# Performance work log

Measured on AMD Instinct MI355X. Metric: run time of the kernel, lower is better.

The kernel has to match this reference:

```python
import jax, jax.numpy as jnp
import numpy as np

B, H, S = 32, 128, 8192

def setup_inputs() -> dict:
    key = jax.random.key(0)
    k1, k2, k3, k4, k5 = jax.random.split(key, 5)
    return {
        "static_hidden": jax.random.normal(k1, (B, H, S), dtype=jnp.float32),
        "dynamic_hidden": jax.random.normal(k2, (B, H, S), dtype=jnp.float32),
        "decoder_hidden": jax.random.normal(k3, (B, H), dtype=jnp.float32),
        "v": jax.random.normal(k4, (1, 1, H), dtype=jnp.float32) * 0.01,
        "W": jax.random.normal(k5, (1, H, 3 * H), dtype=jnp.float32) * 0.01,
    }

def reference(static_hidden, dynamic_hidden, decoder_hidden, v, W):
    b, h, s = static_hidden.shape
    # concat (static, dynamic, expanded decoder) along feature dim -> [b, 3h, s]
    hidden = jnp.concatenate(
        [static_hidden, dynamic_hidden,
         jnp.broadcast_to(decoder_hidden[:, :, None], (b, h, s))], axis=1)
    # W[0]: [h, 3h]; tanh(W @ hidden) -> [b, h, s]
    e = jnp.tanh(jnp.einsum('hk,bks->bhs', W[0], hidden))
    # v[0,0]: [h]; scores -> [b, 1, s]
    scores = jnp.einsum('h,bhs->bs', v[0, 0], e)[:, None, :]
    return jax.nn.softmax(scores, axis=2)
```

## Files before the change

kernel.cpp:

```cpp
#include <hip/hip_runtime.h>
#include <math.h>

#define BB 32
#define HH 128
#define SS 8192

typedef __attribute__((ext_vector_type(8))) short bf8;
typedef __attribute__((ext_vector_type(4))) float f4;

static __device__ __forceinline__ unsigned short f2bf(float x) {
  union { float f; unsigned int u; } c; c.f = x;
  unsigned int r = c.u + 0x7FFFu + ((c.u >> 16) & 1u);
  return (unsigned short)(r >> 16);
}

__global__ __launch_bounds__(256) void prep_kernel(
    const float* __restrict__ W, const float* __restrict__ dec,
    unsigned short* __restrict__ Abf, float* __restrict__ bias) {
  const int b = blockIdx.x;
  const int tid = threadIdx.x;
  if (tid < HH) {
    const float* wr = W + (size_t)tid * 384 + 256;
    const float* db = dec + (size_t)b * HH;
    float acc = 0.f;
    #pragma unroll 8
    for (int j = 0; j < HH; ++j) acc += wr[j] * db[j];
    bias[b * HH + tid] = acc;
  }
  if (b == 0) {
    for (int idx = tid; idx < HH * 256; idx += 256) {
      int h = idx >> 8, k = idx & 255;
      Abf[idx] = f2bf(W[h * 384 + k]);
    }
  }
}

__global__ __launch_bounds__(512, 4) void attn_main(
    const float* __restrict__ sta, const float* __restrict__ dyn,
    const unsigned short* __restrict__ Abf, const float* __restrict__ bias,
    const float* __restrict__ v, float* __restrict__ scores) {
  __shared__ unsigned short LA[128 * 256];

  const int tid  = threadIdx.x;
  const int l    = tid & 63;
  const int quad = l >> 4;
  const int n16  = l & 15;
  const int gw   = (blockIdx.x << 3) + (tid >> 6);
  const int b    = gw >> 9;
  const int tile = gw & 511;
  const int s0   = tile << 4;

  #pragma unroll
  for (int j = 0; j < 8; ++j) {
    int gc = (j << 9) + tid;
    int m = gc >> 5, ck = gc & 31;
    bf8 val = *(const bf8*)(Abf + ((size_t)gc << 3));
    *(bf8*)&LA[m * 256 + ((ck ^ (m & 7)) << 3)] = val;
  }
  __syncthreads();

  const size_t base = ((size_t)b << 20) + (size_t)(quad << 3) * SS + s0 + n16;
  const float* p0 = sta + base;
  const float* p1 = dyn + base;

  f4 acc[8];
  #pragma unroll
  for (int mt = 0; mt < 8; ++mt) acc[mt] = (f4){0.f, 0.f, 0.f, 0.f};

  float tmp[8];
  bf8 cur;

  auto issueB = [&](int step) {
    const float* tp = (step < 4 ? p0 : p1) + ((size_t)((step & 3) << 5)) * SS;
    #pragma unroll
    for (int j = 0; j < 8; ++j)
      tmp[j] = tp[(size_t)j * SS];
  };
  auto conv = [&]() {
    #pragma unroll
    for (int j = 0; j < 8; ++j) cur[j] = (short)f2bf(tmp[j]);
  };

  const int swz = n16 & 7;
  issueB(0);
  conv();
  #pragma unroll
  for (int step = 0; step < 8; ++step) {
    if (step < 7) issueB(step + 1);
    const int koff = (((step << 2) + quad) ^ swz) << 3;
    #pragma unroll
    for (int mt = 0; mt < 8; ++mt) {
      bf8 af = *(const bf8*)&LA[(((mt << 4) + n16) << 8) + koff];
      acc[mt] = __builtin_amdgcn_mfma_f32_16x16x32_bf16(af, cur, acc[mt], 0, 0, 0);
    }
    if (step < 7) conv();
  }

  float part = 0.f;
  #pragma unroll
  for (int mt = 0; mt < 8; ++mt) {
    #pragma unroll
    for (int r = 0; r < 4; ++r) {
      const int h = mt * 16 + quad * 4 + r;
      part += v[h] * tanhf(acc[mt][r] + bias[(b << 7) + h]);
    }
  }
  part += __shfl_xor(part, 16, 64);
  part += __shfl_xor(part, 32, 64);
  if (quad == 0)
    scores[((size_t)b << 13) + s0 + n16] = part;
}

__global__ __launch_bounds__(1024) void softmax_kernel(float* __restrict__ out) {
  const int b = blockIdx.x;
  const int tid = threadIdx.x;
  float* row = out + ((size_t)b << 13);
  float4 x0 = ((const float4*)row)[tid];
  float4 x1 = ((const float4*)row)[tid + 1024];
  float lmax = fmaxf(fmaxf(fmaxf(x0.x, x0.y), fmaxf(x0.z, x0.w)),
                     fmaxf(fmaxf(x1.x, x1.y), fmaxf(x1.z, x1.w)));
  __shared__ float red[17];
  #pragma unroll
  for (int o = 32; o >= 1; o >>= 1) lmax = fmaxf(lmax, __shfl_xor(lmax, o, 64));
  if ((tid & 63) == 0) red[tid >> 6] = lmax;
  __syncthreads();
  if (tid < 64) {
    float m = (tid < 16) ? red[tid] : -3.0e38f;
    #pragma unroll
    for (int o = 8; o >= 1; o >>= 1) m = fmaxf(m, __shfl_xor(m, o, 64));
    if (tid == 0) red[16] = m;
  }
  __syncthreads();
  const float gmax = red[16];
  float e[8];
  e[0] = expf(x0.x - gmax); e[1] = expf(x0.y - gmax);
  e[2] = expf(x0.z - gmax); e[3] = expf(x0.w - gmax);
  e[4] = expf(x1.x - gmax); e[5] = expf(x1.y - gmax);
  e[6] = expf(x1.z - gmax); e[7] = expf(x1.w - gmax);
  float ls = e[0] + e[1] + e[2] + e[3] + e[4] + e[5] + e[6] + e[7];
  #pragma unroll
  for (int o = 32; o >= 1; o >>= 1) ls += __shfl_xor(ls, o, 64);
  __syncthreads();
  if ((tid & 63) == 0) red[tid >> 6] = ls;
  __syncthreads();
  if (tid < 64) {
    float m = (tid < 16) ? red[tid] : 0.f;
    #pragma unroll
    for (int o = 8; o >= 1; o >>= 1) m += __shfl_xor(m, o, 64);
    if (tid == 0) red[16] = m;
  }
  __syncthreads();
  const float inv = 1.0f / red[16];
  float4 o0 = make_float4(e[0] * inv, e[1] * inv, e[2] * inv, e[3] * inv);
  float4 o1 = make_float4(e[4] * inv, e[5] * inv, e[6] * inv, e[7] * inv);
  ((float4*)row)[tid] = o0;
  ((float4*)row)[tid + 1024] = o1;
}

extern "C" void kernel_launch(void* const* d_in, const int* in_sizes, int n_in,
                              void* d_out, int out_size, void* d_ws, size_t ws_size,
                              hipStream_t stream) {
  const float* sta = (const float*)d_in[0];
  const float* dyn = (const float*)d_in[1];
  const float* dec = (const float*)d_in[2];
  const float* v   = (const float*)d_in[3];
  const float* W   = (const float*)d_in[4];

  unsigned short* Abf = (unsigned short*)d_ws;
  float* bias = (float*)((char*)d_ws + 128 * 256 * 2);
  float* scores = (float*)d_out;

  prep_kernel<<<BB, 256, 0, stream>>>(W, dec, Abf, bias);
  attn_main<<<BB * (SS / 16) / 8, 512, 0, stream>>>(sta, dyn, Abf, bias, v, scores);
  softmax_kernel<<<BB, 1024, 0, stream>>>(scores);
}
```

Before: 330.9 us.

## Stage activations through double-buffered LDS with vectorized float4 loads

The main kernel now uses 1024-thread blocks, each covering 256 sequence positions. Activations are loaded as float4 vectors, converted to bf16 and written into a swizzled, double-buffered LDS tile, replacing the earlier per-lane scalar strided global loads. MFMA B operands are then read from LDS, with the next chunk's global loads overlapping the current chunk's compute. The cost is 128KB of dynamic shared memory per block, which limits occupancy to one block per CU, plus a block-wide barrier on every chunk.

```diff
diff --git a/kernel.cpp b/kernel.cpp
--- a/kernel.cpp
+++ b/kernel.cpp
@@ -35,65 +35,80 @@
   }
 }
 
-__global__ __launch_bounds__(512, 4) void attn_main(
+__global__ __launch_bounds__(1024, 4) void attn_main(
     const float* __restrict__ sta, const float* __restrict__ dyn,
     const unsigned short* __restrict__ Abf, const float* __restrict__ bias,
     const float* __restrict__ v, float* __restrict__ scores) {
-  __shared__ unsigned short LA[128 * 256];
+  extern __shared__ __align__(16) unsigned short smem[];
+  unsigned short* LA = smem;
+  unsigned short* LX = smem + 32768;
 
   const int tid  = threadIdx.x;
   const int l    = tid & 63;
+  const int w    = tid >> 6;
   const int quad = l >> 4;
   const int n16  = l & 15;
-  const int gw   = (blockIdx.x << 3) + (tid >> 6);
-  const int b    = gw >> 9;
-  const int tile = gw & 511;
-  const int s0   = tile << 4;
+  const int b     = blockIdx.x >> 5;
+  const int s_blk = (blockIdx.x & 31) << 8;
 
+  const int kq = ((w >> 2) << 4) + (quad << 2);
+  const int sl = ((w & 3) << 6) + (n16 << 2);
+  const size_t gxoff = ((size_t)b * HH) * SS + s_blk + sl;
+
+  f4 g[4];
+  auto issueX = [&](int c) {
+    const float* p = (c < 2 ? sta : dyn) + gxoff + (size_t)(((c & 1) << 6) + kq) * SS;
+    #pragma unroll
+    for (int j = 0; j < 4; ++j) g[j] = *(const f4*)(p + (size_t)j * SS);
+  };
+  auto convWrite = [&](int buf) {
+    unsigned short* X = LX + (buf << 14);
+    #pragma unroll
+    for (int i = 0; i < 4; ++i) {
+      const int srow = sl + i;
+      ushort4 o;
+      o.x = f2bf(g[0][i]); o.y = f2bf(g[1][i]);
+      o.z = f2bf(g[2][i]); o.w = f2bf(g[3][i]);
+      *(ushort4*)&X[(srow << 6) + ((((kq >> 3) ^ (srow & 7)) << 3) | (kq & 7))] = o;
+    }
+  };
+
+  issueX(0);
   #pragma unroll
-  for (int j = 0; j < 8; ++j) {
-    int gc = (j << 9) + tid;
+  for (int j = 0; j < 4; ++j) {
+    int gc = (j << 10) + tid;
     int m = gc >> 5, ck = gc & 31;
     bf8 val = *(const bf8*)(Abf + ((size_t)gc << 3));
-    *(bf8*)&LA[m * 256 + ((ck ^ (m & 7)) << 3)] = val;
+    *(bf8*)&LA[(m << 8) + ((ck ^ (m & 7)) << 3)] = val;
   }
+  convWrite(0);
   __syncthreads();
-
-  const size_t base = ((size_t)b << 20) + (size_t)(quad << 3) * SS + s0 + n16;
-  const float* p0 = sta + base;
-  const float* p1 = dyn + base;
 
   f4 acc[8];
   #pragma unroll
   for (int mt = 0; mt < 8; ++mt) acc[mt] = (f4){0.f, 0.f, 0.f, 0.f};
 
-  float tmp[8];
-  bf8 cur;
+  const int srow = (w << 4) + n16;
+  const int xrow = srow << 6;
+  const int sswz = srow & 7;
+  const int aswz = n16 & 7;
 
-  auto issueB = [&](int step) {
-    const float* tp = (step < 4 ? p0 : p1) + ((size_t)((step & 3) << 5)) * SS;
-    #pragma unroll
-    for (int j = 0; j < 8; ++j)
-      tmp[j] = tp[(size_t)j * SS];
-  };
-  auto conv = [&]() {
-    #pragma unroll
-    for (int j = 0; j < 8; ++j) cur[j] = (short)f2bf(tmp[j]);
-  };
-
-  const int swz = n16 & 7;
-  issueB(0);
-  conv();
   #pragma unroll
-  for (int step = 0; step < 8; ++step) {
-    if (step < 7) issueB(step + 1);
-    const int koff = (((step << 2) + quad) ^ swz) << 3;
+  for (int c = 0; c < 4; ++c) {
+    if (c < 3) issueX(c + 1);
+    const unsigned short* X = LX + ((c & 1) << 14);
+    bf8 bf0 = *(const bf8*)&X[xrow + ((quad ^ sswz) << 3)];
+    bf8 bf1 = *(const bf8*)&X[xrow + (((4 + quad) ^ sswz) << 3)];
     #pragma unroll
     for (int mt = 0; mt < 8; ++mt) {
-      bf8 af = *(const bf8*)&LA[(((mt << 4) + n16) << 8) + koff];
-      acc[mt] = __builtin_amdgcn_mfma_f32_16x16x32_bf16(af, cur, acc[mt], 0, 0, 0);
+      const int arow = (mt << 4) + n16;
+      bf8 a0 = *(const bf8*)&LA[(arow << 8) + ((((c << 3) + quad) ^ aswz) << 3)];
+      acc[mt] = __builtin_amdgcn_mfma_f32_16x16x32_bf16(a0, bf0, acc[mt], 0, 0, 0);
+      bf8 a1 = *(const bf8*)&LA[(arow << 8) + ((((c << 3) + 4 + quad) ^ aswz) << 3)];
+      acc[mt] = __builtin_amdgcn_mfma_f32_16x16x32_bf16(a1, bf1, acc[mt], 0, 0, 0);
     }
-    if (step < 7) conv();
+    if (c < 3) convWrite((c + 1) & 1);
+    __syncthreads();
   }
 
   float part = 0.f;
@@ -101,14 +116,14 @@
   for (int mt = 0; mt < 8; ++mt) {
     #pragma unroll
     for (int r = 0; r < 4; ++r) {
-      const int h = mt * 16 + quad * 4 + r;
+      const int h = (mt << 4) + (quad << 2) + r;
       part += v[h] * tanhf(acc[mt][r] + bias[(b << 7) + h]);
     }
   }
   part += __shfl_xor(part, 16, 64);
   part += __shfl_xor(part, 32, 64);
   if (quad == 0)
-    scores[((size_t)b << 13) + s0 + n16] = part;
+    scores[((size_t)b << 13) + s_blk + srow] = part;
 }
 
 __global__ __launch_bounds__(1024) void softmax_kernel(float* __restrict__ out) {
@@ -170,7 +185,14 @@
   float* bias = (float*)((char*)d_ws + 128 * 256 * 2);
   float* scores = (float*)d_out;
 
+  static bool attr_done = false;
+  if (!attr_done) {
+    (void)hipFuncSetAttribute((const void*)attn_main,
+                              hipFuncAttributeMaxDynamicSharedMemorySize, 131072);
+    attr_done = true;
+  }
+
   prep_kernel<<<BB, 256, 0, stream>>>(W, dec, Abf, bias);
-  attn_main<<<BB * (SS / 16) / 8, 512, 0, stream>>>(sta, dyn, Abf, bias, v, scores);
+  attn_main<<<BB * 32, 1024, 131072, stream>>>(sta, dyn, Abf, bias, v, scores);
   softmax_kernel<<<BB, 1024, 0, stream>>>(scores);
 }
```

After: 327.6 us. No clear change (-1.0%).
